# Optimization experiments

Measured on AMD Instinct MI355X. Metric: run time of the kernel, lower is better.

## Reference

```python
import jax, jax.numpy as jnp
import numpy as np

N_LEVELS = 9

def _avg_pool_2x2(x):
    # tf.nn.avg_pool2d(ksize=2, strides=2, padding='SAME'); H,W even at every
    # level for H=W=512, so SAME == VALID == simple 2x2 mean.
    b, h, w, c = x.shape
    return x.reshape(b, h // 2, 2, w // 2, 2, c).mean(axis=(2, 4))

def setup_inputs() -> dict:
    key = jax.random.key(0)
    x = jax.random.normal(key, (8, 512, 512, 2), dtype=jnp.float32)
    return {"x": x}

def reference(x):
    B, H, W, C = x.shape
    levels = [x]
    cur = x
    for _ in range(N_LEVELS - 1):
        cur = _avg_pool_2x2(cur)
        levels.append(cur)
    # tf.image.resize bilinear (half-pixel centers, no antialias on upsample)
    # == jax.image.resize method='bilinear' for upscaling.
    ups = [jax.image.resize(lv, (B, H, W, C), method='bilinear') for lv in levels]
    stacked = jnp.concatenate(ups, axis=-1)          # [B, H, W, 9*C]
    stacked = stacked[:, None]                       # [B, 1, H, W, 9*C]
    return jnp.transpose(stacked, (0, 4, 2, 3, 1))   # [B, 9*C, H, W, 1]
```

## Files before the change

kernel.cpp:

```cpp
#include <hip/hip_runtime.h>


#define HWTOT (512 * 512)

typedef float vfloat4 __attribute__((ext_vector_type(4)));

__constant__ int c_off2[7] = {0, 0, 524288, 655360, 688128, 696320, 698368};

__global__ __launch_bounds__(256) void build_levels_1_6(const float* __restrict__ x,
                                                        float2* __restrict__ pyr) {
  const int b = blockIdx.y;
  const int tx = blockIdx.x & 7, ty = blockIdx.x >> 3;
  const int t = threadIdx.x;

  __shared__ float2 sh1[32 * 32];
  __shared__ float2 sh2[16 * 16];
  __shared__ float2 sh3[8 * 8];
  __shared__ float2 sh4[4 * 4];
  __shared__ float2 sh5[2 * 2];

  {
    const int i = t >> 3;
    const int j0 = (t & 7) << 2;
    const float* r0 = x + (((size_t)(b * 512 + ty * 64 + 2 * i)) * 512 + (tx * 64 + 2 * j0)) * 2;
    const float* r1 = r0 + 1024;
    float2 o[4];
#pragma unroll
    for (int k = 0; k < 4; ++k) {
      float4 a = *(const float4*)(r0 + 4 * k);
      float4 c = *(const float4*)(r1 + 4 * k);
      o[k].x = (a.x + a.z + c.x + c.z) * 0.25f;
      o[k].y = (a.y + a.w + c.y + c.w) * 0.25f;
      sh1[i * 32 + j0 + k] = o[k];
    }
    float2* g = pyr + ((size_t)(b * 256 + ty * 32 + i) * 256 + tx * 32 + j0);
    *(float4*)(g) = make_float4(o[0].x, o[0].y, o[1].x, o[1].y);
    *(float4*)(g + 2) = make_float4(o[2].x, o[2].y, o[3].x, o[3].y);
  }
  __syncthreads();
  {
    const int i = t >> 4, j = t & 15;
    float2 a = sh1[(2 * i) * 32 + 2 * j], c = sh1[(2 * i) * 32 + 2 * j + 1];
    float2 d = sh1[(2 * i + 1) * 32 + 2 * j], e = sh1[(2 * i + 1) * 32 + 2 * j + 1];
    float2 o = {(a.x + c.x + d.x + e.x) * 0.25f, (a.y + c.y + d.y + e.y) * 0.25f};
    sh2[i * 16 + j] = o;
    pyr[524288 + (size_t)(b * 128 + ty * 16 + i) * 128 + tx * 16 + j] = o;
  }
  __syncthreads();
  if (t < 64) {
    const int i = t >> 3, j = t & 7;
    float2 a = sh2[(2 * i) * 16 + 2 * j], c = sh2[(2 * i) * 16 + 2 * j + 1];
    float2 d = sh2[(2 * i + 1) * 16 + 2 * j], e = sh2[(2 * i + 1) * 16 + 2 * j + 1];
    float2 o = {(a.x + c.x + d.x + e.x) * 0.25f, (a.y + c.y + d.y + e.y) * 0.25f};
    sh3[i * 8 + j] = o;
    pyr[655360 + (size_t)(b * 64 + ty * 8 + i) * 64 + tx * 8 + j] = o;
  }
  __syncthreads();
  if (t < 16) {
    const int i = t >> 2, j = t & 3;
    float2 a = sh3[(2 * i) * 8 + 2 * j], c = sh3[(2 * i) * 8 + 2 * j + 1];
    float2 d = sh3[(2 * i + 1) * 8 + 2 * j], e = sh3[(2 * i + 1) * 8 + 2 * j + 1];
    float2 o = {(a.x + c.x + d.x + e.x) * 0.25f, (a.y + c.y + d.y + e.y) * 0.25f};
    sh4[i * 4 + j] = o;
    pyr[688128 + (size_t)(b * 32 + ty * 4 + i) * 32 + tx * 4 + j] = o;
  }
  __syncthreads();
  if (t < 4) {
    const int i = t >> 1, j = t & 1;
    float2 a = sh4[(2 * i) * 4 + 2 * j], c = sh4[(2 * i) * 4 + 2 * j + 1];
    float2 d = sh4[(2 * i + 1) * 4 + 2 * j], e = sh4[(2 * i + 1) * 4 + 2 * j + 1];
    float2 o = {(a.x + c.x + d.x + e.x) * 0.25f, (a.y + c.y + d.y + e.y) * 0.25f};
    sh5[i * 2 + j] = o;
    pyr[696320 + (size_t)(b * 16 + ty * 2 + i) * 16 + tx * 2 + j] = o;
  }
  __syncthreads();
  if (t == 0) {
    float2 a = sh5[0], c = sh5[1], d = sh5[2], e = sh5[3];
    float2 o = {(a.x + c.x + d.x + e.x) * 0.25f, (a.y + c.y + d.y + e.y) * 0.25f};
    pyr[698368 + (size_t)(b * 8 + ty) * 8 + tx] = o;
  }
}

__global__ __launch_bounds__(256) void upsample_lv(const float* __restrict__ x,
                                                   const float2* __restrict__ pyr,
                                                   float* __restrict__ out) {
  const int t = threadIdx.x;
  const int w0pix = (t & 127) << 2;
  const int h = (blockIdx.x << 1) + (t >> 7);
  const int b = blockIdx.y;
  const int lv = blockIdx.z;
  const size_t obase = (size_t)(b * 18 + 2 * lv) * HWTOT + (size_t)h * 512 + w0pix;

  if (lv == 0) {
    const float* px = x + (((size_t)b * 512 + h) * 512 + w0pix) * 2;
    float4 a = *(const float4*)px;
    float4 c = *(const float4*)(px + 4);
    *(vfloat4*)(out + obase) = (vfloat4){a.x, a.z, c.x, c.z};
    *(vfloat4*)(out + obase + HWTOT) = (vfloat4){a.y, a.w, c.y, c.w};
    return;
  }

  __shared__ float2 stage[20];

  const int S = 512 >> lv;
  const float scale = 1.0f / (float)(1 << lv);

  const float2* img;
  if (lv <= 6) {
    img = pyr + c_off2[lv] + (size_t)b * S * S;
  } else {
    const float2* l6 = pyr + 698368 + (size_t)b * 64;
    if (t < 16) {
      const int i = t >> 2, j = t & 3;
      float2 a = l6[(2 * i) * 8 + 2 * j], c = l6[(2 * i) * 8 + 2 * j + 1];
      float2 d = l6[(2 * i + 1) * 8 + 2 * j], e = l6[(2 * i + 1) * 8 + 2 * j + 1];
      stage[t] = {(a.x + c.x + d.x + e.x) * 0.25f, (a.y + c.y + d.y + e.y) * 0.25f};
    }
    __syncthreads();
    if (lv == 8 && t < 4) {
      const int i = t >> 1, j = t & 1;
      float2 a = stage[(2 * i) * 4 + 2 * j], c = stage[(2 * i) * 4 + 2 * j + 1];
      float2 d = stage[(2 * i + 1) * 4 + 2 * j], e = stage[(2 * i + 1) * 4 + 2 * j + 1];
      stage[16 + t] = {(a.x + c.x + d.x + e.x) * 0.25f, (a.y + c.y + d.y + e.y) * 0.25f};
    }
    __syncthreads();
    img = (lv == 7) ? (const float2*)stage : (const float2*)(stage + 16);
  }

  float sh = ((float)h + 0.5f) * scale - 0.5f;
  float fh0f = floorf(sh);
  float fh = sh - fh0f;
  int h0 = (int)fh0f;
  int h0c = h0 < 0 ? 0 : h0;
  int h1c = (h0 + 1 > S - 1) ? (S - 1) : (h0 + 1);
  const float2* R0 = img + (size_t)h0c * S;
  const float2* R1 = img + (size_t)h1c * S;
  const float wy0 = 1.0f - fh;

  float o0[4], o1[4];
#pragma unroll
  for (int k = 0; k < 4; ++k) {
    float sw = ((float)(w0pix + k) + 0.5f) * scale - 0.5f;
    float fw0f = floorf(sw);
    float fw = sw - fw0f;
    int w0 = (int)fw0f;
    int w0c = w0 < 0 ? 0 : w0;
    int w1c = (w0 + 1 > S - 1) ? (S - 1) : (w0 + 1);
    float2 v00 = R0[w0c], v01 = R0[w1c];
    float2 v10 = R1[w0c], v11 = R1[w1c];
    float wx0 = 1.0f - fw;
    float tx_ = v00.x * wx0 + v01.x * fw;
    float bx_ = v10.x * wx0 + v11.x * fw;
    float ty_ = v00.y * wx0 + v01.y * fw;
    float by_ = v10.y * wx0 + v11.y * fw;
    o0[k] = tx_ * wy0 + bx_ * fh;
    o1[k] = ty_ * wy0 + by_ * fh;
  }
  *(vfloat4*)(out + obase) = (vfloat4){o0[0], o0[1], o0[2], o0[3]};
  *(vfloat4*)(out + obase + HWTOT) = (vfloat4){o1[0], o1[1], o1[2], o1[3]};
}

extern "C" void kernel_launch(void* const* d_in, const int* in_sizes, int n_in,
                              void* d_out, int out_size, void* d_ws, size_t ws_size,
                              hipStream_t stream) {
  const float* x = (const float*)d_in[0];
  float* out = (float*)d_out;
  float2* pyr = (float2*)d_ws;

  build_levels_1_6<<<dim3(64, 8), 256, 0, stream>>>(x, pyr);
  upsample_lv<<<dim3(256, 8, 9), 256, 0, stream>>>(x, pyr, out);
}
```

Measured before the change: 175.7 us.

## Fuse level-0 copy into pyramid build and stage upsample source rows in LDS

The level-0 channel de-interleave is moved into the pyramid-building kernel, which already reads x, so the upsample kernel no longer reads x a second time and drops one grid z slice. The upsample kernel now cooperatively loads the three source rows each block needs into shared memory and samples from LDS instead of issuing gathered global loads. This adds a barrier and per-block row loading, and lengthens the small 64x8-block first kernel with extra output writes, which could expose that kernel's low parallelism.

Measured after the change: 162.7 us. -7.4%, faster.

```diff
diff --git a/kernel.cpp b/kernel.cpp
--- a/kernel.cpp
+++ b/kernel.cpp
@@ -8,7 +8,8 @@
 __constant__ int c_off2[7] = {0, 0, 524288, 655360, 688128, 696320, 698368};
 
 __global__ __launch_bounds__(256) void build_levels_1_6(const float* __restrict__ x,
-                                                        float2* __restrict__ pyr) {
+                                                        float2* __restrict__ pyr,
+                                                        float* __restrict__ out) {
   const int b = blockIdx.y;
   const int tx = blockIdx.x & 7, ty = blockIdx.x >> 3;
   const int t = threadIdx.x;
@@ -22,20 +23,33 @@
   {
     const int i = t >> 3;
     const int j0 = (t & 7) << 2;
-    const float* r0 = x + (((size_t)(b * 512 + ty * 64 + 2 * i)) * 512 + (tx * 64 + 2 * j0)) * 2;
+    const int row0 = ty * 64 + 2 * i;
+    const int colx = tx * 64 + 2 * j0;
+    const float* r0 = x + (((size_t)(b * 512 + row0)) * 512 + colx) * 2;
     const float* r1 = r0 + 1024;
+    float4 a[4], c[4];
     float2 o[4];
 #pragma unroll
     for (int k = 0; k < 4; ++k) {
-      float4 a = *(const float4*)(r0 + 4 * k);
-      float4 c = *(const float4*)(r1 + 4 * k);
-      o[k].x = (a.x + a.z + c.x + c.z) * 0.25f;
-      o[k].y = (a.y + a.w + c.y + c.w) * 0.25f;
+      a[k] = *(const float4*)(r0 + 4 * k);
+      c[k] = *(const float4*)(r1 + 4 * k);
+      o[k].x = (a[k].x + a[k].z + c[k].x + c[k].z) * 0.25f;
+      o[k].y = (a[k].y + a[k].w + c[k].y + c[k].w) * 0.25f;
       sh1[i * 32 + j0 + k] = o[k];
     }
     float2* g = pyr + ((size_t)(b * 256 + ty * 32 + i) * 256 + tx * 32 + j0);
     *(float4*)(g) = make_float4(o[0].x, o[0].y, o[1].x, o[1].y);
     *(float4*)(g + 2) = make_float4(o[2].x, o[2].y, o[3].x, o[3].y);
+
+    const size_t ob = (size_t)(b * 18) * HWTOT + (size_t)row0 * 512 + colx;
+    *(vfloat4*)(out + ob)                  = (vfloat4){a[0].x, a[0].z, a[1].x, a[1].z};
+    *(vfloat4*)(out + ob + 4)              = (vfloat4){a[2].x, a[2].z, a[3].x, a[3].z};
+    *(vfloat4*)(out + ob + 512)            = (vfloat4){c[0].x, c[0].z, c[1].x, c[1].z};
+    *(vfloat4*)(out + ob + 512 + 4)        = (vfloat4){c[2].x, c[2].z, c[3].x, c[3].z};
+    *(vfloat4*)(out + ob + HWTOT)          = (vfloat4){a[0].y, a[0].w, a[1].y, a[1].w};
+    *(vfloat4*)(out + ob + HWTOT + 4)      = (vfloat4){a[2].y, a[2].w, a[3].y, a[3].w};
+    *(vfloat4*)(out + ob + HWTOT + 512)    = (vfloat4){c[0].y, c[0].w, c[1].y, c[1].w};
+    *(vfloat4*)(out + ob + HWTOT + 512 + 4)= (vfloat4){c[2].y, c[2].w, c[3].y, c[3].w};
   }
   __syncthreads();
   {
@@ -81,62 +95,72 @@
   }
 }
 
-__global__ __launch_bounds__(256) void upsample_lv(const float* __restrict__ x,
-                                                   const float2* __restrict__ pyr,
+__global__ __launch_bounds__(256) void upsample_lv(const float2* __restrict__ pyr,
                                                    float* __restrict__ out) {
   const int t = threadIdx.x;
   const int w0pix = (t & 127) << 2;
-  const int h = (blockIdx.x << 1) + (t >> 7);
+  const int dr = t >> 7;
+  const int h = (blockIdx.x << 1) + dr;
   const int b = blockIdx.y;
-  const int lv = blockIdx.z;
+  const int lv = blockIdx.z + 1;
   const size_t obase = (size_t)(b * 18 + 2 * lv) * HWTOT + (size_t)h * 512 + w0pix;
 
-  if (lv == 0) {
-    const float* px = x + (((size_t)b * 512 + h) * 512 + w0pix) * 2;
-    float4 a = *(const float4*)px;
-    float4 c = *(const float4*)(px + 4);
-    *(vfloat4*)(out + obase) = (vfloat4){a.x, a.z, c.x, c.z};
-    *(vfloat4*)(out + obase + HWTOT) = (vfloat4){a.y, a.w, c.y, c.w};
-    return;
-  }
-
-  __shared__ float2 stage[20];
+  __shared__ float2 rows[3 * 256];
 
   const int S = 512 >> lv;
   const float scale = 1.0f / (float)(1 << lv);
 
-  const float2* img;
+  int ldsR0, ldsR1;
+  float fh;
+
   if (lv <= 6) {
-    img = pyr + c_off2[lv] + (size_t)b * S * S;
+    const float hb_e = ((float)(blockIdx.x << 1) + 0.5f) * scale - 0.5f;
+    const int hbase = (int)floorf(hb_e);
+    const int shl = 9 - lv;
+    for (int idx = t; idx < 3 * S; idx += 256) {
+      int r = idx >> shl;
+      int wc = idx & (S - 1);
+      int sr = hbase + r;
+      sr = sr < 0 ? 0 : (sr > S - 1 ? S - 1 : sr);
+      rows[idx] = pyr[c_off2[lv] + (size_t)b * S * S + (size_t)sr * S + wc];
+    }
+    __syncthreads();
+    const float sh = ((float)h + 0.5f) * scale - 0.5f;
+    const float f0 = floorf(sh);
+    fh = sh - f0;
+    const int d0 = (int)f0 - hbase;
+    ldsR0 = d0 * S;
+    ldsR1 = ldsR0 + S;
   } else {
     const float2* l6 = pyr + 698368 + (size_t)b * 64;
     if (t < 16) {
       const int i = t >> 2, j = t & 3;
       float2 a = l6[(2 * i) * 8 + 2 * j], c = l6[(2 * i) * 8 + 2 * j + 1];
       float2 d = l6[(2 * i + 1) * 8 + 2 * j], e = l6[(2 * i + 1) * 8 + 2 * j + 1];
-      stage[t] = {(a.x + c.x + d.x + e.x) * 0.25f, (a.y + c.y + d.y + e.y) * 0.25f};
+      rows[t] = {(a.x + c.x + d.x + e.x) * 0.25f, (a.y + c.y + d.y + e.y) * 0.25f};
     }
     __syncthreads();
-    if (lv == 8 && t < 4) {
-      const int i = t >> 1, j = t & 1;
-      float2 a = stage[(2 * i) * 4 + 2 * j], c = stage[(2 * i) * 4 + 2 * j + 1];
-      float2 d = stage[(2 * i + 1) * 4 + 2 * j], e = stage[(2 * i + 1) * 4 + 2 * j + 1];
-      stage[16 + t] = {(a.x + c.x + d.x + e.x) * 0.25f, (a.y + c.y + d.y + e.y) * 0.25f};
+    if (lv == 8) {
+      if (t < 4) {
+        const int i = t >> 1, j = t & 1;
+        float2 a = rows[(2 * i) * 4 + 2 * j], c = rows[(2 * i) * 4 + 2 * j + 1];
+        float2 d = rows[(2 * i + 1) * 4 + 2 * j], e = rows[(2 * i + 1) * 4 + 2 * j + 1];
+        rows[16 + t] = {(a.x + c.x + d.x + e.x) * 0.25f, (a.y + c.y + d.y + e.y) * 0.25f};
+      }
+      __syncthreads();
     }
-    __syncthreads();
-    img = (lv == 7) ? (const float2*)stage : (const float2*)(stage + 16);
+    const int off = (lv == 7) ? 0 : 16;
+    const float sh = ((float)h + 0.5f) * scale - 0.5f;
+    const float f0 = floorf(sh);
+    fh = sh - f0;
+    int h0 = (int)f0;
+    int h0c = h0 < 0 ? 0 : h0;
+    int h1c = (h0 + 1 > S - 1) ? (S - 1) : (h0 + 1);
+    ldsR0 = off + h0c * S;
+    ldsR1 = off + h1c * S;
   }
 
-  float sh = ((float)h + 0.5f) * scale - 0.5f;
-  float fh0f = floorf(sh);
-  float fh = sh - fh0f;
-  int h0 = (int)fh0f;
-  int h0c = h0 < 0 ? 0 : h0;
-  int h1c = (h0 + 1 > S - 1) ? (S - 1) : (h0 + 1);
-  const float2* R0 = img + (size_t)h0c * S;
-  const float2* R1 = img + (size_t)h1c * S;
   const float wy0 = 1.0f - fh;
-
   float o0[4], o1[4];
 #pragma unroll
   for (int k = 0; k < 4; ++k) {
@@ -146,8 +170,8 @@
     int w0 = (int)fw0f;
     int w0c = w0 < 0 ? 0 : w0;
     int w1c = (w0 + 1 > S - 1) ? (S - 1) : (w0 + 1);
-    float2 v00 = R0[w0c], v01 = R0[w1c];
-    float2 v10 = R1[w0c], v11 = R1[w1c];
+    float2 v00 = rows[ldsR0 + w0c], v01 = rows[ldsR0 + w1c];
+    float2 v10 = rows[ldsR1 + w0c], v11 = rows[ldsR1 + w1c];
     float wx0 = 1.0f - fw;
     float tx_ = v00.x * wx0 + v01.x * fw;
     float bx_ = v10.x * wx0 + v11.x * fw;
@@ -167,6 +191,6 @@
   float* out = (float*)d_out;
   float2* pyr = (float2*)d_ws;
 
-  build_levels_1_6<<<dim3(64, 8), 256, 0, stream>>>(x, pyr);
-  upsample_lv<<<dim3(256, 8, 9), 256, 0, stream>>>(x, pyr, out);
+  build_levels_1_6<<<dim3(64, 8), 256, 0, stream>>>(x, pyr, out);
+  upsample_lv<<<dim3(256, 8, 8), 256, 0, stream>>>(pyr, out);
 }
```

## Fuse level-0 copy into pyramid build and stage source rows in LDS for upsampling

Applied to the files above, without the earlier changes.

The level-0 output copy now happens inside a new first-stage kernel that reads x once, writes the level-1 pool and transposes the input into the output. The upsample kernel then handles levels 1 through 8, producing four output rows per block from clamped source rows staged in shared memory with a one-pixel halo. Level 1 gets a specialised path with constant 0.25/0.75 weights. The level-2 to level-6 build now reads level 1 back from the workspace, which adds a third launch and an extra round trip through global memory.

New measurement: 166.8 us. -5.1%, faster.

```diff
diff --git a/kernel.cpp b/kernel.cpp
--- a/kernel.cpp
+++ b/kernel.cpp
@@ -2,13 +2,41 @@
 
 
 #define HWTOT (512 * 512)
+#define RW 260
 
 typedef float vfloat4 __attribute__((ext_vector_type(4)));
 
 __constant__ int c_off2[7] = {0, 0, 524288, 655360, 688128, 696320, 698368};
 
-__global__ __launch_bounds__(256) void build_levels_1_6(const float* __restrict__ x,
-                                                        float2* __restrict__ pyr) {
+__global__ __launch_bounds__(256) void build_lv01(const float* __restrict__ x,
+                                                  float2* __restrict__ pyr,
+                                                  float* __restrict__ out) {
+  const int b = blockIdx.y;
+  const int tx = blockIdx.x & 7;
+  const int ty = blockIdx.x >> 3;
+  const int t = threadIdx.x;
+  const int i = t >> 4;
+  const int j = t & 15;
+  const int xr = ty * 32 + 2 * i;
+  const int xc = tx * 64 + 4 * j;
+  const float* r0 = x + ((size_t)(b * 512 + xr) * 512 + xc) * 2;
+  const float* r1 = r0 + 1024;
+  float4 a0 = *(const float4*)r0;
+  float4 a1 = *(const float4*)(r0 + 4);
+  float4 c0 = *(const float4*)r1;
+  float4 c1 = *(const float4*)(r1 + 4);
+  float2 o0 = {(a0.x + a0.z + c0.x + c0.z) * 0.25f, (a0.y + a0.w + c0.y + c0.w) * 0.25f};
+  float2 o1 = {(a1.x + a1.z + c1.x + c1.z) * 0.25f, (a1.y + a1.w + c1.y + c1.w) * 0.25f};
+  float2* g = pyr + ((size_t)(b * 256 + ty * 16 + i) * 256 + tx * 32 + 2 * j);
+  *(vfloat4*)g = (vfloat4){o0.x, o0.y, o1.x, o1.y};
+  const size_t ob = (size_t)(b * 18) * HWTOT + (size_t)xr * 512 + xc;
+  *(vfloat4*)(out + ob) = (vfloat4){a0.x, a0.z, a1.x, a1.z};
+  *(vfloat4*)(out + ob + 512) = (vfloat4){c0.x, c0.z, c1.x, c1.z};
+  *(vfloat4*)(out + ob + HWTOT) = (vfloat4){a0.y, a0.w, a1.y, a1.w};
+  *(vfloat4*)(out + ob + HWTOT + 512) = (vfloat4){c0.y, c0.w, c1.y, c1.w};
+}
+
+__global__ __launch_bounds__(256) void build_lv2_6(float2* pyr) {
   const int b = blockIdx.y;
   const int tx = blockIdx.x & 7, ty = blockIdx.x >> 3;
   const int t = threadIdx.x;
@@ -20,22 +48,12 @@
   __shared__ float2 sh5[2 * 2];
 
   {
-    const int i = t >> 3;
-    const int j0 = (t & 7) << 2;
-    const float* r0 = x + (((size_t)(b * 512 + ty * 64 + 2 * i)) * 512 + (tx * 64 + 2 * j0)) * 2;
-    const float* r1 = r0 + 1024;
-    float2 o[4];
-#pragma unroll
-    for (int k = 0; k < 4; ++k) {
-      float4 a = *(const float4*)(r0 + 4 * k);
-      float4 c = *(const float4*)(r1 + 4 * k);
-      o[k].x = (a.x + a.z + c.x + c.z) * 0.25f;
-      o[k].y = (a.y + a.w + c.y + c.w) * 0.25f;
-      sh1[i * 32 + j0 + k] = o[k];
-    }
-    float2* g = pyr + ((size_t)(b * 256 + ty * 32 + i) * 256 + tx * 32 + j0);
-    *(float4*)(g) = make_float4(o[0].x, o[0].y, o[1].x, o[1].y);
-    *(float4*)(g + 2) = make_float4(o[2].x, o[2].y, o[3].x, o[3].y);
+    const int row = t >> 3, c4 = (t & 7) << 2;
+    const float2* src = pyr + (size_t)(b * 256 + ty * 32 + row) * 256 + tx * 32 + c4;
+    float4 v0 = *(const float4*)src;
+    float4 v1 = *(const float4*)(src + 2);
+    *(float4*)&sh1[t * 4] = v0;
+    *(float4*)&sh1[t * 4 + 2] = v1;
   }
   __syncthreads();
   {
@@ -81,83 +99,141 @@
   }
 }
 
-__global__ __launch_bounds__(256) void upsample_lv(const float* __restrict__ x,
-                                                   const float2* __restrict__ pyr,
+__global__ __launch_bounds__(256) void upsample_lv(const float2* __restrict__ pyr,
                                                    float* __restrict__ out) {
   const int t = threadIdx.x;
-  const int w0pix = (t & 127) << 2;
-  const int h = (blockIdx.x << 1) + (t >> 7);
+  const int tp = t & 127;
+  const int rr0 = t >> 7;
+  const int w0pix = tp << 2;
+  const int bx = blockIdx.x;
   const int b = blockIdx.y;
-  const int lv = blockIdx.z;
-  const size_t obase = (size_t)(b * 18 + 2 * lv) * HWTOT + (size_t)h * 512 + w0pix;
-
-  if (lv == 0) {
-    const float* px = x + (((size_t)b * 512 + h) * 512 + w0pix) * 2;
-    float4 a = *(const float4*)px;
-    float4 c = *(const float4*)(px + 4);
-    *(vfloat4*)(out + obase) = (vfloat4){a.x, a.z, c.x, c.z};
-    *(vfloat4*)(out + obase + HWTOT) = (vfloat4){a.y, a.w, c.y, c.w};
-    return;
-  }
-
-  __shared__ float2 stage[20];
-
+  const int lv = blockIdx.z + 1;
   const int S = 512 >> lv;
   const float scale = 1.0f / (float)(1 << lv);
 
-  const float2* img;
+  __shared__ float2 rows[4 * RW + 20];
+
+  const int W = S + 2;
+  const int hbase = (int)floorf(((float)(bx << 2) + 0.5f) * scale - 0.5f);
+
   if (lv <= 6) {
-    img = pyr + c_off2[lv] + (size_t)b * S * S;
+#pragma unroll
+    for (int r = 0; r < 4; ++r) {
+      int sr = hbase + r;
+      sr = sr < 0 ? 0 : (sr > S - 1 ? S - 1 : sr);
+      const float2* src = pyr + c_off2[lv] + (size_t)b * S * S + (size_t)sr * S;
+      for (int c = t; c < W; c += 256) {
+        int sc = c - 1;
+        sc = sc < 0 ? 0 : (sc > S - 1 ? S - 1 : sc);
+        rows[r * RW + c] = src[sc];
+      }
+    }
   } else {
+    float2* img7 = rows + 4 * RW;
+    float2* img8 = img7 + 16;
     const float2* l6 = pyr + 698368 + (size_t)b * 64;
     if (t < 16) {
       const int i = t >> 2, j = t & 3;
       float2 a = l6[(2 * i) * 8 + 2 * j], c = l6[(2 * i) * 8 + 2 * j + 1];
       float2 d = l6[(2 * i + 1) * 8 + 2 * j], e = l6[(2 * i + 1) * 8 + 2 * j + 1];
-      stage[t] = {(a.x + c.x + d.x + e.x) * 0.25f, (a.y + c.y + d.y + e.y) * 0.25f};
+      img7[t] = {(a.x + c.x + d.x + e.x) * 0.25f, (a.y + c.y + d.y + e.y) * 0.25f};
     }
     __syncthreads();
     if (lv == 8 && t < 4) {
       const int i = t >> 1, j = t & 1;
-      float2 a = stage[(2 * i) * 4 + 2 * j], c = stage[(2 * i) * 4 + 2 * j + 1];
-      float2 d = stage[(2 * i + 1) * 4 + 2 * j], e = stage[(2 * i + 1) * 4 + 2 * j + 1];
-      stage[16 + t] = {(a.x + c.x + d.x + e.x) * 0.25f, (a.y + c.y + d.y + e.y) * 0.25f};
+      float2 a = img7[(2 * i) * 4 + 2 * j], c = img7[(2 * i) * 4 + 2 * j + 1];
+      float2 d = img7[(2 * i + 1) * 4 + 2 * j], e = img7[(2 * i + 1) * 4 + 2 * j + 1];
+      img8[t] = {(a.x + c.x + d.x + e.x) * 0.25f, (a.y + c.y + d.y + e.y) * 0.25f};
     }
     __syncthreads();
-    img = (lv == 7) ? (const float2*)stage : (const float2*)(stage + 16);
-  }
-
-  float sh = ((float)h + 0.5f) * scale - 0.5f;
-  float fh0f = floorf(sh);
-  float fh = sh - fh0f;
-  int h0 = (int)fh0f;
-  int h0c = h0 < 0 ? 0 : h0;
-  int h1c = (h0 + 1 > S - 1) ? (S - 1) : (h0 + 1);
-  const float2* R0 = img + (size_t)h0c * S;
-  const float2* R1 = img + (size_t)h1c * S;
-  const float wy0 = 1.0f - fh;
-
-  float o0[4], o1[4];
+    const float2* img = (lv == 7) ? img7 : img8;
+    if (t < 4 * W) {
+      int r, c;
+      if (lv == 7) {
+        r = t / 6;
+        c = t - r * 6;
+      } else {
+        r = t >> 2;
+        c = t & 3;
+      }
+      int sr = hbase + r;
+      sr = sr < 0 ? 0 : (sr > S - 1 ? S - 1 : sr);
+      int sc = c - 1;
+      sc = sc < 0 ? 0 : (sc > S - 1 ? S - 1 : sc);
+      rows[r * RW + c] = img[sr * S + sc];
+    }
+  }
+  __syncthreads();
+
+  const size_t obase0 =
+      (size_t)(b * 18 + 2 * lv) * HWTOT + (size_t)((bx << 2) + rr0) * 512 + w0pix;
+
+  if (lv == 1) {
+    const int e0 = tp << 1;
+#pragma unroll
+    for (int dr2 = 0; dr2 < 2; ++dr2) {
+      const int rr = rr0 + 2 * dr2;
+      const int d0 = (rr + 1) >> 1;
+      const float fh = (rr & 1) ? 0.25f : 0.75f;
+      const float wy0 = 1.0f - fh;
+      const float2* R0 = rows + d0 * RW + e0;
+      const float2* R1 = R0 + RW;
+      float2 p0 = R0[0], p1 = R0[1], p2 = R0[2], p3 = R0[3];
+      float2 q0 = R1[0], q1 = R1[1], q2 = R1[2], q3 = R1[3];
+      float hx0 = p0.x * 0.25f + p1.x * 0.75f, hy0 = p0.y * 0.25f + p1.y * 0.75f;
+      float hx1 = p1.x * 0.75f + p2.x * 0.25f, hy1 = p1.y * 0.75f + p2.y * 0.25f;
+      float hx2 = p1.x * 0.25f + p2.x * 0.75f, hy2 = p1.y * 0.25f + p2.y * 0.75f;
+      float hx3 = p2.x * 0.75f + p3.x * 0.25f, hy3 = p2.y * 0.75f + p3.y * 0.25f;
+      float gx0 = q0.x * 0.25f + q1.x * 0.75f, gy0 = q0.y * 0.25f + q1.y * 0.75f;
+      float gx1 = q1.x * 0.75f + q2.x * 0.25f, gy1 = q1.y * 0.75f + q2.y * 0.25f;
+      float gx2 = q1.x * 0.25f + q2.x * 0.75f, gy2 = q1.y * 0.25f + q2.y * 0.75f;
+      float gx3 = q2.x * 0.75f + q3.x * 0.25f, gy3 = q2.y * 0.75f + q3.y * 0.25f;
+      const size_t ob = obase0 + (size_t)dr2 * 1024;
+      *(vfloat4*)(out + ob) = (vfloat4){hx0 * wy0 + gx0 * fh, hx1 * wy0 + gx1 * fh,
+                                        hx2 * wy0 + gx2 * fh, hx3 * wy0 + gx3 * fh};
+      *(vfloat4*)(out + ob + HWTOT) = (vfloat4){hy0 * wy0 + gy0 * fh, hy1 * wy0 + gy1 * fh,
+                                                hy2 * wy0 + gy2 * fh, hy3 * wy0 + gy3 * fh};
+    }
+    return;
+  }
+
+  int w0l[4];
+  float fw[4];
 #pragma unroll
   for (int k = 0; k < 4; ++k) {
     float sw = ((float)(w0pix + k) + 0.5f) * scale - 0.5f;
-    float fw0f = floorf(sw);
-    float fw = sw - fw0f;
-    int w0 = (int)fw0f;
-    int w0c = w0 < 0 ? 0 : w0;
-    int w1c = (w0 + 1 > S - 1) ? (S - 1) : (w0 + 1);
-    float2 v00 = R0[w0c], v01 = R0[w1c];
-    float2 v10 = R1[w0c], v11 = R1[w1c];
-    float wx0 = 1.0f - fw;
-    float tx_ = v00.x * wx0 + v01.x * fw;
-    float bx_ = v10.x * wx0 + v11.x * fw;
-    float ty_ = v00.y * wx0 + v01.y * fw;
-    float by_ = v10.y * wx0 + v11.y * fw;
-    o0[k] = tx_ * wy0 + bx_ * fh;
-    o1[k] = ty_ * wy0 + by_ * fh;
-  }
-  *(vfloat4*)(out + obase) = (vfloat4){o0[0], o0[1], o0[2], o0[3]};
-  *(vfloat4*)(out + obase + HWTOT) = (vfloat4){o1[0], o1[1], o1[2], o1[3]};
+    float f = floorf(sw);
+    fw[k] = sw - f;
+    w0l[k] = (int)f + 1;
+  }
+#pragma unroll
+  for (int dr2 = 0; dr2 < 2; ++dr2) {
+    const int rr = rr0 + 2 * dr2;
+    const int h = (bx << 2) + rr;
+    float shf = ((float)h + 0.5f) * scale - 0.5f;
+    float f0 = floorf(shf);
+    float fh = shf - f0;
+    int d0 = (int)f0 - hbase;
+    const float2* R0 = rows + d0 * RW;
+    const float2* R1 = R0 + RW;
+    const float wy0 = 1.0f - fh;
+    float o0[4], o1[4];
+#pragma unroll
+    for (int k = 0; k < 4; ++k) {
+      float2 v00 = R0[w0l[k]], v01 = R0[w0l[k] + 1];
+      float2 v10 = R1[w0l[k]], v11 = R1[w0l[k] + 1];
+      float wx0 = 1.0f - fw[k];
+      float tx_ = v00.x * wx0 + v01.x * fw[k];
+      float bx_ = v10.x * wx0 + v11.x * fw[k];
+      float ty_ = v00.y * wx0 + v01.y * fw[k];
+      float by_ = v10.y * wx0 + v11.y * fw[k];
+      o0[k] = tx_ * wy0 + bx_ * fh;
+      o1[k] = ty_ * wy0 + by_ * fh;
+    }
+    const size_t ob = obase0 + (size_t)dr2 * 1024;
+    *(vfloat4*)(out + ob) = (vfloat4){o0[0], o0[1], o0[2], o0[3]};
+    *(vfloat4*)(out + ob + HWTOT) = (vfloat4){o1[0], o1[1], o1[2], o1[3]};
+  }
 }
 
 extern "C" void kernel_launch(void* const* d_in, const int* in_sizes, int n_in,
@@ -167,6 +243,7 @@
   float* out = (float*)d_out;
   float2* pyr = (float2*)d_ws;
 
-  build_levels_1_6<<<dim3(64, 8), 256, 0, stream>>>(x, pyr);
-  upsample_lv<<<dim3(256, 8, 9), 256, 0, stream>>>(x, pyr, out);
-}
+  build_lv01<<<dim3(128, 8), 256, 0, stream>>>(x, pyr, out);
+  build_lv2_6<<<dim3(64, 8), 256, 0, stream>>>(pyr);
+  upsample_lv<<<dim3(128, 8, 8), 256, 0, stream>>>(pyr, out);
+}
```
